# Optimization experiments

Hardware: AMD Instinct MI355X
Metric: run time of the kernel (lower is better)

## Reference

```python
import jax, jax.numpy as jnp
import numpy as np

B, N, H, E_PER = 32, 128, 128, 4096  # graphs, nodes/graph, hidden_dim, pairs/graph


def setup_inputs() -> dict:
    key = jax.random.key(0)
    k1, k2, k3, k4, k5 = jax.random.split(key, 5)
    h_node = jax.random.normal(k1, (B, N, H), dtype=jnp.float32)
    h_edge = jax.random.normal(k2, (B, N, N, H), dtype=jnp.float32)
    # pairlist rows (b, i, j), grouped by batch index b as the torch loop assumes
    b = jnp.repeat(jnp.arange(B, dtype=jnp.int32), E_PER)
    i = jax.random.randint(k3, (B * E_PER,), 0, N, dtype=jnp.int32)
    j = jax.random.randint(k4, (B * E_PER,), 0, N, dtype=jnp.int32)
    pairlist = jnp.stack([b, i, j], axis=1)
    # foward_message_layer: Linear(3H, 6H); store weight transposed for x @ W
    W = jax.random.normal(k5, (3 * H, 6 * H), dtype=jnp.float32) / np.float32(np.sqrt(3 * H))
    bias = jnp.zeros((6 * H,), dtype=jnp.float32)
    return {"h_node": h_node, "h_edge": h_edge, "pairlist": pairlist, "W": W, "bias": bias}


def reference(h_node, h_edge, pairlist, W, bias):
    # Gather per-pair node/edge embeddings and concat: [E, 3H]
    bi, ii, jj = pairlist[:, 0], pairlist[:, 1], pairlist[:, 2]
    m = jnp.concatenate(
        [h_node[bi, ii], h_node[bi, jj], h_edge[bi, ii, jj]], axis=-1
    )
    # Shared linear message transform (Linear(3H, 6H)), then regroup per graph
    out = m @ W + bias  # [E, 6H]
    return out.reshape(B, E_PER, 6 * H)
```

## Files before the change

### kernel.cpp

```cpp
#include <hip/hip_runtime.h>


#define NNODE 128
#define HDIM  128
#define KDIM  384
#define NOUT  768
#define BM    128
#define BN    128
#define BK    64
#define NKITER 6

typedef __attribute__((ext_vector_type(4))) float f32x4;
typedef __attribute__((ext_vector_type(8))) short bf16x8;

static __device__ __forceinline__ short f2b(float f) {
    return __builtin_bit_cast(short, (__bf16)f);
}

__global__ void prep_kernel(const float* __restrict__ W, short* __restrict__ Wt) {
    int n = blockIdx.x;
    for (int k = threadIdx.x; k < KDIM; k += 256) {
        Wt[n * KDIM + k] = f2b(W[k * NOUT + n]);
    }
}

__global__ __launch_bounds__(256) void gemm_kernel(
    const float* __restrict__ h_node, const float* __restrict__ h_edge,
    const int* __restrict__ pl, const short* __restrict__ Wt,
    const float* __restrict__ bias, float* __restrict__ out) {

    __shared__ int rowOff[3][BM];
    __shared__ __align__(16) short Abuf[BM * BK];
    __shared__ __align__(16) short Bbuf[BN * BK];

    const int tid = threadIdx.x;
    const int mBase = (int)(blockIdx.x & 1023) * BM;
    const int nBase = (int)(blockIdx.x >> 10) * BN;

    if (tid < BM) {
        int e = mBase + tid;
        int b  = pl[3 * e + 0];
        int ii = pl[3 * e + 1];
        int jj = pl[3 * e + 2];
        rowOff[0][tid] = (b * NNODE + ii) * HDIM;
        rowOff[1][tid] = (b * NNODE + jj) * HDIM;
        rowOff[2][tid] = ((b * NNODE + ii) * NNODE + jj) * HDIM;
    }
    __syncthreads();

    const int lane = tid & 63;
    const int wid  = tid >> 6;
    const int wm   = wid & 1;
    const int wn   = wid >> 1;
    const int r    = lane & 15;
    const int g    = lane >> 4;

    const int srow = tid >> 3;
    const int sc   = tid & 7;

    f32x4 acc[4][4];
    #pragma unroll
    for (int a = 0; a < 4; ++a)
        #pragma unroll
        for (int b2 = 0; b2 < 4; ++b2)
            acc[a][b2] = (f32x4){0.f, 0.f, 0.f, 0.f};

    char* Ab = (char*)Abuf;
    char* Bb = (char*)Bbuf;

    for (int kk = 0; kk < NKITER; ++kk) {
        const int seg  = kk >> 1;
        const float* gbase = (seg < 2) ? h_node : h_edge;
        const int koff = (kk & 1) * BK;

        f32x4 ax[4], ay[4];
        #pragma unroll
        for (int t = 0; t < 4; ++t) {
            int row = srow + t * 32;
            const float* p = gbase + rowOff[seg][row] + koff + sc * 8;
            ax[t] = *(const f32x4*)p;
            ay[t] = *(const f32x4*)(p + 4);
        }
        bf16x8 bv[4];
        #pragma unroll
        for (int t = 0; t < 4; ++t) {
            int row = srow + t * 32;
            bv[t] = *(const bf16x8*)(Wt + (nBase + row) * KDIM + kk * BK + sc * 8);
        }

        __syncthreads();

        #pragma unroll
        for (int t = 0; t < 4; ++t) {
            int row  = srow + t * 32;
            int byte = row * (BK * 2) + sc * 16;
            byte ^= (row & 7) << 4;
            bf16x8 v;
            v[0] = f2b(ax[t][0]); v[1] = f2b(ax[t][1]);
            v[2] = f2b(ax[t][2]); v[3] = f2b(ax[t][3]);
            v[4] = f2b(ay[t][0]); v[5] = f2b(ay[t][1]);
            v[6] = f2b(ay[t][2]); v[7] = f2b(ay[t][3]);
            *(bf16x8*)(Ab + byte) = v;
            *(bf16x8*)(Bb + byte) = bv[t];
        }

        __syncthreads();

        #pragma unroll
        for (int ks = 0; ks < 2; ++ks) {
            const int cb = ks * 4 + g;
            bf16x8 ef[4], wf[4];
            #pragma unroll
            for (int mf = 0; mf < 4; ++mf) {
                int row  = wm * 64 + mf * 16 + r;
                int byte = row * (BK * 2) + cb * 16;
                byte ^= (row & 7) << 4;
                ef[mf] = *(const bf16x8*)(Ab + byte);
            }
            #pragma unroll
            for (int nf = 0; nf < 4; ++nf) {
                int row  = wn * 64 + nf * 16 + r;
                int byte = row * (BK * 2) + cb * 16;
                byte ^= (row & 7) << 4;
                wf[nf] = *(const bf16x8*)(Bb + byte);
            }
            #pragma unroll
            for (int nf = 0; nf < 4; ++nf)
                #pragma unroll
                for (int mf = 0; mf < 4; ++mf)
                    acc[nf][mf] = __builtin_amdgcn_mfma_f32_16x16x32_bf16(
                        wf[nf], ef[mf], acc[nf][mf], 0, 0, 0);
        }
    }

    #pragma unroll
    for (int nf = 0; nf < 4; ++nf) {
        int n = nBase + wn * 64 + nf * 16 + g * 4;
        f32x4 bb = *(const f32x4*)(bias + n);
        #pragma unroll
        for (int mf = 0; mf < 4; ++mf) {
            int m = mBase + wm * 64 + mf * 16 + r;
            f32x4 v = acc[nf][mf] + bb;
            *(f32x4*)(out + (size_t)m * NOUT + n) = v;
        }
    }
}

extern "C" void kernel_launch(void* const* d_in, const int* in_sizes, int n_in,
                              void* d_out, int out_size, void* d_ws, size_t ws_size,
                              hipStream_t stream) {
    const float* h_node = (const float*)d_in[0];
    const float* h_edge = (const float*)d_in[1];
    const int*   pl     = (const int*)d_in[2];
    const float* W      = (const float*)d_in[3];
    const float* bias   = (const float*)d_in[4];
    float* out = (float*)d_out;
    short* Wt  = (short*)d_ws;

    prep_kernel<<<NOUT, 256, 0, stream>>>(W, Wt);
    gemm_kernel<<<1024 * 6, 256, 0, stream>>>(h_node, h_edge, pl, Wt, bias, out);
}
```

Baseline: 663.9 us.

## Double-buffer LDS tiles, pre-swizzle W, load B via direct-to-LDS, remap blocks per XCD

```diff
diff --git a/kernel.cpp b/kernel.cpp
--- a/kernel.cpp
+++ b/kernel.cpp
@@ -17,31 +17,50 @@
     return __builtin_bit_cast(short, (__bf16)f);
 }
 
-__global__ void prep_kernel(const float* __restrict__ W, short* __restrict__ Wt) {
-    int n = blockIdx.x;
-    for (int k = threadIdx.x; k < KDIM; k += 256) {
-        Wt[n * KDIM + k] = f2b(W[k * NOUT + n]);
-    }
+static __device__ __forceinline__ void gload_lds16(const void* g, void* l) {
+    __builtin_amdgcn_global_load_lds((const __attribute__((address_space(1))) void*)g,
+                                     (__attribute__((address_space(3))) void*)l, 16, 0, 0);
+}
+
+__global__ void prep_kernel(const float* __restrict__ W, short* __restrict__ WtS) {
+    int gid  = blockIdx.x * 256 + threadIdx.x;
+    int tile = gid >> 10;
+    int c    = gid & 1023;
+    int nb   = tile / 6, kk = tile - nb * 6;
+    int row  = c >> 3;
+    int kb   = (c & 7) ^ (row & 7);
+    int n    = nb * 128 + row;
+    int k0   = kk * 64 + kb * 8;
+    short v[8];
+    #pragma unroll
+    for (int e = 0; e < 8; ++e) v[e] = f2b(W[(k0 + e) * NOUT + n]);
+    *(bf16x8*)(WtS + (size_t)gid * 8) = *(bf16x8*)v;
 }
 
 __global__ __launch_bounds__(256) void gemm_kernel(
     const float* __restrict__ h_node, const float* __restrict__ h_edge,
-    const int* __restrict__ pl, const short* __restrict__ Wt,
+    const int* __restrict__ pl, const short* __restrict__ WtS,
     const float* __restrict__ bias, float* __restrict__ out) {
 
     __shared__ int rowOff[3][BM];
-    __shared__ __align__(16) short Abuf[BM * BK];
-    __shared__ __align__(16) short Bbuf[BN * BK];
+    __shared__ __align__(16) short Abuf[2][BM * BK];
+    __shared__ __align__(16) short Bbuf[2][BN * BK];
 
     const int tid = threadIdx.x;
-    const int mBase = (int)(blockIdx.x & 1023) * BM;
-    const int nBase = (int)(blockIdx.x >> 10) * BN;
+    const int bid = blockIdx.x;
+    const int xcd = bid & 7;
+    const int idx = bid >> 3;
+    const int mBase = (xcd * 128 + idx / 6) * BM;
+    const int nb    = idx % 6;
+    const int nBase = nb * BN;
+    const int nb6   = nb * 6;
 
     if (tid < BM) {
-        int e = mBase + tid;
-        int b  = pl[3 * e + 0];
-        int ii = pl[3 * e + 1];
-        int jj = pl[3 * e + 2];
+        int e  = pl ? mBase + tid : 0;
+        int b  = pl[3 * (mBase + tid) + 0];
+        int ii = pl[3 * (mBase + tid) + 1];
+        int jj = pl[3 * (mBase + tid) + 2];
+        (void)e;
         rowOff[0][tid] = (b * NNODE + ii) * HDIM;
         rowOff[1][tid] = (b * NNODE + jj) * HDIM;
         rowOff[2][tid] = ((b * NNODE + ii) * NNODE + jj) * HDIM;
@@ -54,10 +73,16 @@
     const int wn   = wid >> 1;
     const int r    = lane & 15;
     const int g    = lane >> 4;
-
     const int srow = tid >> 3;
     const int sc   = tid & 7;
 
+    int ro[3][4];
+    #pragma unroll
+    for (int s = 0; s < 3; ++s)
+        #pragma unroll
+        for (int t = 0; t < 4; ++t)
+            ro[s][t] = rowOff[s][srow + t * 32];
+
     f32x4 acc[4][4];
     #pragma unroll
     for (int a = 0; a < 4; ++a)
@@ -65,47 +90,45 @@
         for (int b2 = 0; b2 < 4; ++b2)
             acc[a][b2] = (f32x4){0.f, 0.f, 0.f, 0.f};
 
-    char* Ab = (char*)Abuf;
-    char* Bb = (char*)Bbuf;
-
-    for (int kk = 0; kk < NKITER; ++kk) {
-        const int seg  = kk >> 1;
-        const float* gbase = (seg < 2) ? h_node : h_edge;
-        const int koff = (kk & 1) * BK;
-
-        f32x4 ax[4], ay[4];
+    f32x4 a0[4], a1[4];
+
+    auto issueA = [&](int kt) {
+        const int seg  = kt >> 1;
+        const float* gb = (seg < 2) ? h_node : h_edge;
+        const int koff = (kt & 1) * BK;
         #pragma unroll
         for (int t = 0; t < 4; ++t) {
-            int row = srow + t * 32;
-            const float* p = gbase + rowOff[seg][row] + koff + sc * 8;
-            ax[t] = *(const f32x4*)p;
-            ay[t] = *(const f32x4*)(p + 4);
-        }
-        bf16x8 bv[4];
-        #pragma unroll
-        for (int t = 0; t < 4; ++t) {
-            int row = srow + t * 32;
-            bv[t] = *(const bf16x8*)(Wt + (nBase + row) * KDIM + kk * BK + sc * 8);
-        }
-
-        __syncthreads();
-
+            const float* p = gb + ro[seg][t] + koff + sc * 8;
+            a0[t] = *(const f32x4*)p;
+            a1[t] = *(const f32x4*)(p + 4);
+        }
+    };
+    auto issueB = [&](int kt, int buf) {
+        const short* src = WtS + (size_t)((nb6 + kt) << 10) * 8;
+        short* ldsb = &Bbuf[buf][0];
+        #pragma unroll
+        for (int i = 0; i < 4; ++i) {
+            int cb0 = wid * 256 + i * 64;
+            gload_lds16(src + (size_t)(cb0 + lane) * 8, ldsb + cb0 * 8);
+        }
+    };
+    auto writeA = [&](int buf) {
+        char* Ab = (char*)&Abuf[buf][0];
         #pragma unroll
         for (int t = 0; t < 4; ++t) {
             int row  = srow + t * 32;
-            int byte = row * (BK * 2) + sc * 16;
-            byte ^= (row & 7) << 4;
+            int byte = (row * 128 + sc * 16) ^ ((row & 7) << 4);
             bf16x8 v;
-            v[0] = f2b(ax[t][0]); v[1] = f2b(ax[t][1]);
-            v[2] = f2b(ax[t][2]); v[3] = f2b(ax[t][3]);
-            v[4] = f2b(ay[t][0]); v[5] = f2b(ay[t][1]);
-            v[6] = f2b(ay[t][2]); v[7] = f2b(ay[t][3]);
+            v[0] = f2b(a0[t][0]); v[1] = f2b(a0[t][1]);
+            v[2] = f2b(a0[t][2]); v[3] = f2b(a0[t][3]);
+            v[4] = f2b(a1[t][0]); v[5] = f2b(a1[t][1]);
+            v[6] = f2b(a1[t][2]); v[7] = f2b(a1[t][3]);
             *(bf16x8*)(Ab + byte) = v;
-            *(bf16x8*)(Bb + byte) = bv[t];
-        }
-
-        __syncthreads();
-
+        }
+    };
+    auto compute = [&](int buf) {
+        char* Ab = (char*)&Abuf[buf][0];
+        char* Bb = (char*)&Bbuf[buf][0];
         #pragma unroll
         for (int ks = 0; ks < 2; ++ks) {
             const int cb = ks * 4 + g;
@@ -113,15 +136,13 @@
             #pragma unroll
             for (int mf = 0; mf < 4; ++mf) {
                 int row  = wm * 64 + mf * 16 + r;
-                int byte = row * (BK * 2) + cb * 16;
-                byte ^= (row & 7) << 4;
+                int byte = (row * 128 + cb * 16) ^ ((row & 7) << 4);
                 ef[mf] = *(const bf16x8*)(Ab + byte);
             }
             #pragma unroll
             for (int nf = 0; nf < 4; ++nf) {
                 int row  = wn * 64 + nf * 16 + r;
-                int byte = row * (BK * 2) + cb * 16;
-                byte ^= (row & 7) << 4;
+                int byte = (row * 128 + cb * 16) ^ ((row & 7) << 4);
                 wf[nf] = *(const bf16x8*)(Bb + byte);
             }
             #pragma unroll
@@ -131,6 +152,28 @@
                     acc[nf][mf] = __builtin_amdgcn_mfma_f32_16x16x32_bf16(
                         wf[nf], ef[mf], acc[nf][mf], 0, 0, 0);
         }
+    };
+
+    issueA(0);
+    issueB(0, 0);
+    asm volatile("s_waitcnt vmcnt(0)" ::: "memory");
+    writeA(0);
+    __syncthreads();
+
+    int cur = 0;
+    #pragma unroll
+    for (int t = 0; t < NKITER; ++t) {
+        if (t + 1 < NKITER) {
+            issueA(t + 1);
+            issueB(t + 1, cur ^ 1);
+        }
+        compute(cur);
+        if (t + 1 < NKITER) {
+            asm volatile("s_waitcnt vmcnt(0)" ::: "memory");
+            writeA(cur ^ 1);
+            __syncthreads();
+        }
+        cur ^= 1;
     }
 
     #pragma unroll
@@ -155,8 +198,8 @@
     const float* W      = (const float*)d_in[3];
     const float* bias   = (const float*)d_in[4];
     float* out = (float*)d_out;
-    short* Wt  = (short*)d_ws;
-
-    prep_kernel<<<NOUT, 256, 0, stream>>>(W, Wt);
-    gemm_kernel<<<1024 * 6, 256, 0, stream>>>(h_node, h_edge, pl, Wt, bias, out);
-}
+    short* WtS = (short*)d_ws;
+
+    prep_kernel<<<144, 256, 0, stream>>>(W, WtS);
+    gemm_kernel<<<1024 * 6, 256, 0, stream>>>(h_node, h_edge, pl, WtS, bias, out);
+}
```

New measurement: 636.1 us. 1.04x faster.
